# Kernel tuning notes

Hardware: AMD Instinct MI355X
Metric: run time of the kernel (lower is better)

Reference implementation:

```python
import jax, jax.numpy as jnp
import numpy as np

B, T, C, H = 16, 2048, 512, 64


def _skew(x):
    # x: (B, T1, T2) -> relative-position skew trick (Music Transformer)
    b, t1, t2 = x.shape
    x = jnp.pad(x, ((0, 0), (0, 0), (1, 0)))        # pad one column on the left
    x = x.reshape(b, t2 + 1, t1)                    # reinterpret layout
    x = x[:, 1:, :]                                 # drop first row
    return jnp.transpose(x, (0, 2, 1))              # (B, T1, T2)


def setup_inputs() -> dict:
    key = jax.random.key(0)
    ks = jax.random.split(key, 5)
    return {
        "x": jax.random.normal(ks[0], (B, T, C), dtype=jnp.float32),
        "Wq": jax.random.normal(ks[1], (C, H), dtype=jnp.float32) * 0.02,
        "Wk": jax.random.normal(ks[2], (C, H), dtype=jnp.float32) * 0.02,
        "Wv": jax.random.normal(ks[3], (C, H), dtype=jnp.float32) * 0.02,
        "Er": jax.random.normal(ks[4], (T, H), dtype=jnp.float32),
    }


def reference(x, Wq, Wk, Wv, Er):
    b, t, c = x.shape
    q = x @ Wq  # (B, T, H)
    k = x @ Wk
    v = x @ Wv
    scale = 1.0 / (k.shape[-1] ** 0.5)
    att = jnp.einsum("bth,bsh->bts", q, k) * scale  # (B, T, T)
    # relative position bias via skew trick
    rel_att = jnp.einsum("bth,rh->btr", q, Er[:t])  # (B, T, T)
    att = att + _skew(rel_att)
    # causal mask
    mask = jnp.tril(jnp.ones((t, t), dtype=bool))
    att = jnp.where(mask, att, -jnp.inf)
    att = jax.nn.softmax(att, axis=-1)
    # dropout is identity in eval mode
    out = att @ v  # (B, T, H)
    return out
```

## Files before the change

kernel.cpp:

```cpp
#include <hip/hip_runtime.h>
#include <hip/hip_bf16.h>

#define TT 2048
#define HB 64
#define NB 16
#define NSPLIT 6

typedef __attribute__((ext_vector_type(8))) short short8;
typedef __attribute__((ext_vector_type(4))) float floatx4;

static __device__ __forceinline__ unsigned short f2bf(float f) {
  __hip_bfloat16 h = __float2bfloat16(f);
  return *reinterpret_cast<unsigned short*>(&h);
}
static __device__ __forceinline__ float bf2f(unsigned short u) {
  __hip_bfloat16 h = *reinterpret_cast<__hip_bfloat16*>(&u);
  return __bfloat162float(h);
}

__global__ __launch_bounds__(256) void prep_kernel(
    const float* __restrict__ Wq, const float* __restrict__ Wk,
    const float* __restrict__ Wv, const float* __restrict__ Er,
    unsigned short* __restrict__ Wt, unsigned short* __restrict__ Erb) {
  const int bx = blockIdx.x, tid = threadIdx.x;
  if (bx < 512) {
    int idx = bx * 256 + tid;
    Erb[idx] = f2bf(Er[idx]);
  } else {
    int n = bx - 512;
    const float* Ws[3] = {Wq, Wk, Wv};
#pragma unroll
    for (int m = 0; m < 3; m++)
      for (int k = tid; k < 512; k += 256)
        Wt[(size_t)(m * 64 + n) * 512 + k] = f2bf(Ws[m][(size_t)k * 64 + n]);
  }
}

__global__ __launch_bounds__(256) void proj_kernel(
    const float* __restrict__ x, const unsigned short* __restrict__ Wt,
    unsigned short* __restrict__ qb, unsigned short* __restrict__ kb,
    unsigned short* __restrict__ vT) {
  const int tid = threadIdx.x;
  const int w = tid >> 6, l = tid & 63, quad = l >> 4, lm = l & 15;
  const int m0 = blockIdx.x * 64;
  const int row_a = m0 + w * 16 + lm;

  floatx4 acc[12];
#pragma unroll
  for (int i = 0; i < 12; i++) acc[i] = (floatx4){0.f, 0.f, 0.f, 0.f};

  auto LDA = [&](short8* af, int kt) {
#pragma unroll
    for (int kc = 0; kc < 2; kc++) {
      const float* px = &x[(size_t)row_a * 512 + kt + kc * 32 + quad * 8];
      float4 f0 = *(const float4*)px;
      float4 f1 = *(const float4*)(px + 4);
      short8 s;
      s[0] = f2bf(f0.x); s[1] = f2bf(f0.y); s[2] = f2bf(f0.z); s[3] = f2bf(f0.w);
      s[4] = f2bf(f1.x); s[5] = f2bf(f1.y); s[6] = f2bf(f1.z); s[7] = f2bf(f1.w);
      af[kc] = s;
    }
  };
  auto MFMAS = [&](const short8* af, int kt) {
#pragma unroll
    for (int nt = 0; nt < 12; nt++) {
      const unsigned short* pw =
          &Wt[(size_t)((nt >> 2) * 64 + (nt & 3) * 16 + lm) * 512 + kt + quad * 8];
      short8 b0 = *(const short8*)pw;
      short8 b1 = *(const short8*)(pw + 32);
      acc[nt] = __builtin_amdgcn_mfma_f32_16x16x32_bf16(af[0], b0, acc[nt], 0, 0, 0);
      acc[nt] = __builtin_amdgcn_mfma_f32_16x16x32_bf16(af[1], b1, acc[nt], 0, 0, 0);
    }
  };

  short8 afA[2], afB[2];
  LDA(afA, 0);
#pragma unroll
  for (int kt = 0; kt < 512; kt += 128) {
    LDA(afB, kt + 64);
    MFMAS(afA, kt);
    if (kt + 128 < 512) LDA(afA, kt + 128);
    MFMAS(afB, kt + 64);
  }

  const int b = m0 >> 11;
#pragma unroll
  for (int nt = 0; nt < 12; nt++) {
    int col = (nt & 3) * 16 + lm;
#pragma unroll
    for (int rg = 0; rg < 4; rg++) {
      int row = m0 + w * 16 + quad * 4 + rg;
      unsigned short hv = f2bf(acc[nt][rg]);
      if (nt < 4) qb[(size_t)row * 64 + col] = hv;
      else if (nt < 8) kb[(size_t)row * 64 + col] = hv;
      else vT[(size_t)(b * 64 + col) * 2048 + (row & 2047)] = hv;
    }
  }
}

#define SLICE_B 10880

__global__ __launch_bounds__(384, 2) void attn_kernel(
    const unsigned short* __restrict__ qb, const unsigned short* __restrict__ kb,
    const unsigned short* __restrict__ vT, const unsigned short* __restrict__ Erb,
    float* __restrict__ out) {
  __shared__ __align__(16) char smem[NSPLIT * SLICE_B];

  const int tid = threadIdx.x;
  const int w = tid >> 6;
  const int lane = tid & 63;
  const int quad = lane >> 4, lm = lane & 15;

  float* Ds = (float*)(smem + w * SLICE_B);
  unsigned short* Ps = (unsigned short*)(smem + w * SLICE_B + 8192);
  float* dbv = (float*)(smem + w * SLICE_B + 8192 + 2560);
  const float* DsL = Ds + lm * 63 + quad * 4;

  const int xcd = blockIdx.x & 7;
  const int slot = blockIdx.x >> 3;
  const int b = xcd + ((slot & 1) << 3);
  const int pr = slot >> 1;
  const int s = w;

  const size_t qoff = (size_t)b * (2048 * 64);
  const unsigned short* qB = qb + qoff;
  const unsigned short* kB = kb + qoff;
  const unsigned short* vB = vT + qoff;

  short8 ebf[2];
#pragma unroll
  for (int kc = 0; kc < 2; kc++) {
    short8 z = (short8){0, 0, 0, 0, 0, 0, 0, 0};
    if (lm == 0)
      z = *(const short8*)&Erb[(size_t)2047 * 64 + kc * 32 + quad * 8];
    ebf[kc] = z;
  }

  for (int ph = 0; ph < 2; ph++) {
    const int it = ph ? (63 - pr) : pr;
    const int i0 = it * 32;

    short8 qf[2][2];
#pragma unroll
    for (int mt = 0; mt < 2; mt++)
#pragma unroll
      for (int kc = 0; kc < 2; kc++)
        qf[mt][kc] =
            *(const short8*)&qB[(size_t)(i0 + mt * 16 + lm) * 64 + kc * 32 + quad * 8];

    if ((it % NSPLIT) == w) {
#pragma unroll
      for (int mt = 0; mt < 2; mt++) {
        floatx4 dacc = (floatx4){0.f, 0.f, 0.f, 0.f};
        dacc = __builtin_amdgcn_mfma_f32_16x16x32_bf16(qf[mt][0], ebf[0], dacc, 0, 0, 0);
        dacc = __builtin_amdgcn_mfma_f32_16x16x32_bf16(qf[mt][1], ebf[1], dacc, 0, 0, 0);
        if (lm == 0) {
#pragma unroll
          for (int rg = 0; rg < 4; rg++)
            dbv[mt * 16 + quad * 4 + rg] = dacc[rg];
        }
      }
    }
    __builtin_amdgcn_wave_barrier();

    floatx4 O[2][4];
#pragma unroll
    for (int mt = 0; mt < 2; mt++)
#pragma unroll
      for (int nt = 0; nt < 4; nt++) O[mt][nt] = (floatx4){0.f, 0.f, 0.f, 0.f};
    float m_st[2][4], l_st[2][4];
#pragma unroll
    for (int mt = 0; mt < 2; mt++)
#pragma unroll
      for (int rg = 0; rg < 4; rg++) { m_st[mt][rg] = -1e30f; l_st[mt][rg] = 0.f; }

    for (int jt = s; jt <= it; jt += NSPLIT) {
      const int j0 = jt * 32;
      const int d = i0 - j0;
      const int e0 = (d - 33 > 0) ? (d - 33) : 0;

      short8 kf[2][2], uf[2][2], ef[4][2], vf[4];
#pragma unroll
      for (int t = 0; t < 2; t++)
#pragma unroll
        for (int kc = 0; kc < 2; kc++)
          kf[t][kc] =
              *(const short8*)&kB[(size_t)(j0 + t * 16 + lm) * 64 + kc * 32 + quad * 8];
#pragma unroll
      for (int ct = 0; ct < 2; ct++)
#pragma unroll
        for (int kc = 0; kc < 2; kc++) {
          int ur = j0 + ct * 16 + lm + 1;
          if (ur > 2047) ur = 2047;
          uf[ct][kc] = *(const short8*)&qB[(size_t)ur * 64 + kc * 32 + quad * 8];
        }
#pragma unroll
      for (int et = 0; et < 4; et++)
#pragma unroll
        for (int kc = 0; kc < 2; kc++)
          ef[et][kc] = *(const short8*)&Erb[(size_t)(e0 + et * 16 + lm) * 64 +
                                            kc * 32 + quad * 8];
#pragma unroll
      for (int nt = 0; nt < 4; nt++)
        vf[nt] = *(const short8*)&vB[(size_t)(nt * 16 + lm) * 2048 + j0 + quad * 8];

      __builtin_amdgcn_wave_barrier();

#pragma unroll
      for (int ct = 0; ct < 2; ct++)
#pragma unroll
        for (int et = 0; et < 4; et++) {
          floatx4 dacc = (floatx4){0.f, 0.f, 0.f, 0.f};
          dacc = __builtin_amdgcn_mfma_f32_16x16x32_bf16(uf[ct][0], ef[et][0], dacc, 0, 0, 0);
          dacc = __builtin_amdgcn_mfma_f32_16x16x32_bf16(uf[ct][1], ef[et][1], dacc, 0, 0, 0);
#pragma unroll
          for (int rg = 0; rg < 4; rg++)
            Ds[(ct * 16 + quad * 4 + rg) * 64 + et * 16 + lm] = dacc[rg];
        }

      floatx4 S[2][2];
#pragma unroll
      for (int mt = 0; mt < 2; mt++)
#pragma unroll
        for (int t = 0; t < 2; t++) {
          floatx4 a = (floatx4){0.f, 0.f, 0.f, 0.f};
          a = __builtin_amdgcn_mfma_f32_16x16x32_bf16(qf[mt][0], kf[t][0], a, 0, 0, 0);
          a = __builtin_amdgcn_mfma_f32_16x16x32_bf16(qf[mt][1], kf[t][1], a, 0, 0, 0);
          S[mt][t] = a;
        }

      __builtin_amdgcn_wave_barrier();
      asm volatile("s_waitcnt lgkmcnt(0)" ::: "memory");
      __builtin_amdgcn_sched_barrier(0);

      float sv0[8], sv1[8], lmx[8];
      bool allok = true;
      if (d >= 64) {
#pragma unroll
        for (int mt = 0; mt < 2; mt++)
#pragma unroll
          for (int rg = 0; rg < 4; rg++) {
            const int c = mt * 4 + rg;
            float d0 = DsL[mt * 16 + rg + 31];
            float d1 = DsL[1008 + mt * 16 + rg + 31];
            sv0[c] = fmaf(0.125f, S[mt][0][rg], d0);
            sv1[c] = fmaf(0.125f, S[mt][1][rg], d1);
            lmx[c] = fmaxf(sv0[c], sv1[c]);
            allok = allok && (lmx[c] <= m_st[mt][rg] + 8.f);
          }
      } else {
#pragma unroll
        for (int mt = 0; mt < 2; mt++)
#pragma unroll
          for (int rg = 0; rg < 4; rg++) {
            const int c = mt * 4 + rg;
            const int rloc = mt * 16 + quad * 4 + rg;
            const int i = i0 + rloc;
            float v0, v1;
            {
              int j = j0 + lm;
              float raw = 0.125f * S[mt][0][rg];
              if (j > i) v0 = -1e30f;
              else if (j == i) v0 = raw + dbv[rloc];
              else if (j == i - 1) v0 = raw;
              else v0 = raw + Ds[lm * 64 + (i - j - 2 - e0)];
            }
            {
              int j = j0 + 16 + lm;
              float raw = 0.125f * S[mt][1][rg];
              if (j > i) v1 = -1e30f;
              else if (j == i) v1 = raw + dbv[rloc];
              else if (j == i - 1) v1 = raw;
              else v1 = raw + Ds[(16 + lm) * 64 + (i - j - 2 - e0)];
            }
            sv0[c] = v0; sv1[c] = v1;
            lmx[c] = fmaxf(v0, v1);
            allok = allok && (lmx[c] <= m_st[mt][rg] + 8.f);
          }
      }

      if (__all((int)allok)) {
#pragma unroll
        for (int mt = 0; mt < 2; mt++)
#pragma unroll
          for (int rg = 0; rg < 4; rg++) {
            const int c = mt * 4 + rg;
            const int rloc = mt * 16 + quad * 4 + rg;
            float p0 = __expf(sv0[c] - m_st[mt][rg]);
            float p1 = __expf(sv1[c] - m_st[mt][rg]);
            l_st[mt][rg] += p0 + p1;
            Ps[rloc * 40 + lm] = f2bf(p0);
            Ps[rloc * 40 + 16 + lm] = f2bf(p1);
          }
      } else {
#pragma unroll
        for (int mt = 0; mt < 2; mt++)
#pragma unroll
          for (int rg = 0; rg < 4; rg++) {
            const int c = mt * 4 + rg;
            const int rloc = mt * 16 + quad * 4 + rg;
            float mx = lmx[c];
            mx = fmaxf(mx, __shfl_xor(mx, 1));
            mx = fmaxf(mx, __shfl_xor(mx, 2));
            mx = fmaxf(mx, __shfl_xor(mx, 4));
            mx = fmaxf(mx, __shfl_xor(mx, 8));
            float m_new = fmaxf(m_st[mt][rg], mx);
            float alpha = __expf(m_st[mt][rg] - m_new);
            float p0 = __expf(sv0[c] - m_new);
            float p1 = __expf(sv1[c] - m_new);
            l_st[mt][rg] = l_st[mt][rg] * alpha + (p0 + p1);
            m_st[mt][rg] = m_new;
#pragma unroll
            for (int nt = 0; nt < 4; nt++) O[mt][nt][rg] *= alpha;
            Ps[rloc * 40 + lm] = f2bf(p0);
            Ps[rloc * 40 + 16 + lm] = f2bf(p1);
          }
      }

      __builtin_amdgcn_wave_barrier();
      asm volatile("s_waitcnt lgkmcnt(0)" ::: "memory");
      __builtin_amdgcn_sched_barrier(0);

#pragma unroll
      for (int mt = 0; mt < 2; mt++) {
        short8 pa = *(const short8*)&Ps[(mt * 16 + lm) * 40 + quad * 8];
#pragma unroll
        for (int nt = 0; nt < 4; nt++)
          O[mt][nt] = __builtin_amdgcn_mfma_f32_16x16x32_bf16(pa, vf[nt], O[mt][nt], 0, 0, 0);
      }
    }

    {
      float* Os = (float*)(smem + w * SLICE_B);
      float* mlm = (float*)(smem + w * SLICE_B + 8320);
      float* mll = (float*)(smem + w * SLICE_B + 8448);
#pragma unroll
      for (int mt = 0; mt < 2; mt++)
#pragma unroll
        for (int rg = 0; rg < 4; rg++) {
          float lr = l_st[mt][rg];
          lr += __shfl_xor(lr, 1);
          lr += __shfl_xor(lr, 2);
          lr += __shfl_xor(lr, 4);
          lr += __shfl_xor(lr, 8);
          const int rloc = mt * 16 + quad * 4 + rg;
          if (lm == 0) { mlm[rloc] = m_st[mt][rg]; mll[rloc] = lr; }
#pragma unroll
          for (int nt = 0; nt < 4; nt++)
            Os[rloc * 65 + nt * 16 + lm] = O[mt][nt][rg];
        }
    }
    __syncthreads();
    if (tid < 256) {
      const int row = tid >> 3, c0 = (tid & 7) * 8;
      float mstar = -1e30f;
#pragma unroll
      for (int s2 = 0; s2 < NSPLIT; s2++)
        mstar = fmaxf(mstar, *(const float*)(smem + s2 * SLICE_B + 8320 + row * 4));
      float den = 0.f;
      float acc[8];
#pragma unroll
      for (int c = 0; c < 8; c++) acc[c] = 0.f;
#pragma unroll
      for (int s2 = 0; s2 < NSPLIT; s2++) {
        const char* sl = smem + s2 * SLICE_B;
        float ms = *(const float*)(sl + 8320 + row * 4);
        float ls = *(const float*)(sl + 8448 + row * 4);
        float a = __expf(ms - mstar);
        den += a * ls;
        const float* osp = (const float*)sl + row * 65 + c0;
#pragma unroll
        for (int c = 0; c < 8; c++) acc[c] += a * osp[c];
      }
      float inv = 1.f / den;
      float4 r0 = {acc[0] * inv, acc[1] * inv, acc[2] * inv, acc[3] * inv};
      float4 r1 = {acc[4] * inv, acc[5] * inv, acc[6] * inv, acc[7] * inv};
      float* po = &out[qoff + (size_t)(i0 + row) * 64 + c0];
      *(float4*)po = r0;
      *((float4*)po + 1) = r1;
    }
    __syncthreads();
  }
}

extern "C" void kernel_launch(void* const* d_in, const int* in_sizes, int n_in,
                              void* d_out, int out_size, void* d_ws,
                              size_t ws_size, hipStream_t stream) {
  const float* x = (const float*)d_in[0];
  const float* Wq = (const float*)d_in[1];
  const float* Wk = (const float*)d_in[2];
  const float* Wv = (const float*)d_in[3];
  const float* Er = (const float*)d_in[4];
  float* out = (float*)d_out;

  unsigned short* qb = (unsigned short*)d_ws;
  unsigned short* kb = qb + 2097152;
  unsigned short* vT = kb + 2097152;
  unsigned short* Wt = vT + 2097152;
  unsigned short* Erb = Wt + 98304;

  prep_kernel<<<576, 256, 0, stream>>>(Wq, Wk, Wv, Er, Wt, Erb);
  proj_kernel<<<512, 256, 0, stream>>>(x, Wt, qb, kb, vT);
  attn_kernel<<<512, 384, 0, stream>>>(qb, kb, vT, Erb, out);
}
```

Baseline: 244.3 us.

## Store relative-bias tile in fp16 and merge splits in two halves to shrink LDS

The per-wave relative-position tile in shared memory is now stored as fp16 instead of fp32. The final cross-split merge of partial outputs is done in two 32-column halves, with an extra barrier between them. Together these cut the per-wave LDS slice from 10880 to 6784 bytes, which may allow more blocks per CU or reduce LDS traffic. The cost is fp16 rounding on the bias values, extra conversion instructions, and an additional synchronisation round in the epilogue.

```diff
diff --git a/kernel.cpp b/kernel.cpp
--- a/kernel.cpp
+++ b/kernel.cpp
@@ -1,5 +1,6 @@
 #include <hip/hip_runtime.h>
 #include <hip/hip_bf16.h>
+#include <hip/hip_fp16.h>
 
 #define TT 2048
 #define HB 64
@@ -16,6 +17,14 @@
 static __device__ __forceinline__ float bf2f(unsigned short u) {
   __hip_bfloat16 h = *reinterpret_cast<__hip_bfloat16*>(&u);
   return __bfloat162float(h);
+}
+static __device__ __forceinline__ unsigned short f2h(float f) {
+  __half h = __float2half(f);
+  return *reinterpret_cast<unsigned short*>(&h);
+}
+static __device__ __forceinline__ float h2f(unsigned short u) {
+  __half h = *reinterpret_cast<__half*>(&u);
+  return __half2float(h);
 }
 
 __global__ __launch_bounds__(256) void prep_kernel(
@@ -98,7 +107,7 @@
   }
 }
 
-#define SLICE_B 10880
+#define SLICE_B 6784
 
 __global__ __launch_bounds__(384, 2) void attn_kernel(
     const unsigned short* __restrict__ qb, const unsigned short* __restrict__ kb,
@@ -111,10 +120,10 @@
   const int lane = tid & 63;
   const int quad = lane >> 4, lm = lane & 15;
 
-  float* Ds = (float*)(smem + w * SLICE_B);
-  unsigned short* Ps = (unsigned short*)(smem + w * SLICE_B + 8192);
-  float* dbv = (float*)(smem + w * SLICE_B + 8192 + 2560);
-  const float* DsL = Ds + lm * 63 + quad * 4;
+  unsigned short* Dsb = (unsigned short*)(smem + w * SLICE_B);
+  unsigned short* Ps = (unsigned short*)(smem + w * SLICE_B + 4096);
+  float* dbv = (float*)(smem + w * SLICE_B + 6656);
+  const unsigned short* DsL16 = Dsb + lm * 63 + quad * 4;
 
   const int xcd = blockIdx.x & 7;
   const int slot = blockIdx.x >> 3;
@@ -215,7 +224,7 @@
           dacc = __builtin_amdgcn_mfma_f32_16x16x32_bf16(uf[ct][1], ef[et][1], dacc, 0, 0, 0);
 #pragma unroll
           for (int rg = 0; rg < 4; rg++)
-            Ds[(ct * 16 + quad * 4 + rg) * 64 + et * 16 + lm] = dacc[rg];
+            Dsb[(ct * 16 + quad * 4 + rg) * 64 + et * 16 + lm] = f2h(dacc[rg]);
         }
 
       floatx4 S[2][2];
@@ -241,8 +250,8 @@
 #pragma unroll
           for (int rg = 0; rg < 4; rg++) {
             const int c = mt * 4 + rg;
-            float d0 = DsL[mt * 16 + rg + 31];
-            float d1 = DsL[1008 + mt * 16 + rg + 31];
+            float d0 = h2f(DsL16[mt * 16 + rg + 31]);
+            float d1 = h2f(DsL16[1008 + mt * 16 + rg + 31]);
             sv0[c] = fmaf(0.125f, S[mt][0][rg], d0);
             sv1[c] = fmaf(0.125f, S[mt][1][rg], d1);
             lmx[c] = fmaxf(sv0[c], sv1[c]);
@@ -263,7 +272,7 @@
               if (j > i) v0 = -1e30f;
               else if (j == i) v0 = raw + dbv[rloc];
               else if (j == i - 1) v0 = raw;
-              else v0 = raw + Ds[lm * 64 + (i - j - 2 - e0)];
+              else v0 = raw + h2f(Dsb[lm * 64 + (i - j - 2 - e0)]);
             }
             {
               int j = j0 + 16 + lm;
@@ -271,7 +280,7 @@
               if (j > i) v1 = -1e30f;
               else if (j == i) v1 = raw + dbv[rloc];
               else if (j == i - 1) v1 = raw;
-              else v1 = raw + Ds[(16 + lm) * 64 + (i - j - 2 - e0)];
+              else v1 = raw + h2f(Dsb[(16 + lm) * 64 + (i - j - 2 - e0)]);
             }
             sv0[c] = v0; sv1[c] = v1;
             lmx[c] = fmaxf(v0, v1);
@@ -330,56 +339,64 @@
       }
     }
 
-    {
-      float* Os = (float*)(smem + w * SLICE_B);
-      float* mlm = (float*)(smem + w * SLICE_B + 8320);
-      float* mll = (float*)(smem + w * SLICE_B + 8448);
-#pragma unroll
-      for (int mt = 0; mt < 2; mt++)
-#pragma unroll
-        for (int rg = 0; rg < 4; rg++) {
-          float lr = l_st[mt][rg];
-          lr += __shfl_xor(lr, 1);
-          lr += __shfl_xor(lr, 2);
-          lr += __shfl_xor(lr, 4);
-          lr += __shfl_xor(lr, 8);
-          const int rloc = mt * 16 + quad * 4 + rg;
-          if (lm == 0) { mlm[rloc] = m_st[mt][rg]; mll[rloc] = lr; }
-#pragma unroll
-          for (int nt = 0; nt < 4; nt++)
-            Os[rloc * 65 + nt * 16 + lm] = O[mt][nt][rg];
+    float lred[2][4];
+#pragma unroll
+    for (int mt = 0; mt < 2; mt++)
+#pragma unroll
+      for (int rg = 0; rg < 4; rg++) {
+        float lr = l_st[mt][rg];
+        lr += __shfl_xor(lr, 1);
+        lr += __shfl_xor(lr, 2);
+        lr += __shfl_xor(lr, 4);
+        lr += __shfl_xor(lr, 8);
+        lred[mt][rg] = lr;
+      }
+#pragma unroll
+    for (int half = 0; half < 2; half++) {
+      {
+        float* Os = (float*)(smem + w * SLICE_B);
+        float* mlm = (float*)(smem + w * SLICE_B + 4608);
+        float* mll = (float*)(smem + w * SLICE_B + 4736);
+#pragma unroll
+        for (int mt = 0; mt < 2; mt++)
+#pragma unroll
+          for (int rg = 0; rg < 4; rg++) {
+            const int rloc = mt * 16 + quad * 4 + rg;
+            if (half == 0 && lm == 0) {
+              mlm[rloc] = m_st[mt][rg];
+              mll[rloc] = lred[mt][rg];
+            }
+#pragma unroll
+            for (int ntl = 0; ntl < 2; ntl++)
+              Os[rloc * 36 + ntl * 16 + lm] = O[mt][half * 2 + ntl][rg];
+          }
+      }
+      __syncthreads();
+      if (tid < 256) {
+        const int row = tid >> 3, c0 = (tid & 7) * 4;
+        float mstar = -1e30f;
+#pragma unroll
+        for (int s2 = 0; s2 < NSPLIT; s2++)
+          mstar = fmaxf(mstar, *(const float*)(smem + s2 * SLICE_B + 4608 + row * 4));
+        float den = 0.f;
+        float acc[4] = {0.f, 0.f, 0.f, 0.f};
+#pragma unroll
+        for (int s2 = 0; s2 < NSPLIT; s2++) {
+          const char* sl = smem + s2 * SLICE_B;
+          float ms = *(const float*)(sl + 4608 + row * 4);
+          float ls = *(const float*)(sl + 4736 + row * 4);
+          float a = __expf(ms - mstar);
+          den += a * ls;
+          const float* osp = (const float*)sl + row * 36 + c0;
+#pragma unroll
+          for (int c = 0; c < 4; c++) acc[c] += a * osp[c];
         }
-    }
-    __syncthreads();
-    if (tid < 256) {
-      const int row = tid >> 3, c0 = (tid & 7) * 8;
-      float mstar = -1e30f;
-#pragma unroll
-      for (int s2 = 0; s2 < NSPLIT; s2++)
-        mstar = fmaxf(mstar, *(const float*)(smem + s2 * SLICE_B + 8320 + row * 4));
-      float den = 0.f;
-      float acc[8];
-#pragma unroll
-      for (int c = 0; c < 8; c++) acc[c] = 0.f;
-#pragma unroll
-      for (int s2 = 0; s2 < NSPLIT; s2++) {
-        const char* sl = smem + s2 * SLICE_B;
-        float ms = *(const float*)(sl + 8320 + row * 4);
-        float ls = *(const float*)(sl + 8448 + row * 4);
-        float a = __expf(ms - mstar);
-        den += a * ls;
-        const float* osp = (const float*)sl + row * 65 + c0;
-#pragma unroll
-        for (int c = 0; c < 8; c++) acc[c] += a * osp[c];
-      }
-      float inv = 1.f / den;
-      float4 r0 = {acc[0] * inv, acc[1] * inv, acc[2] * inv, acc[3] * inv};
-      float4 r1 = {acc[4] * inv, acc[5] * inv, acc[6] * inv, acc[7] * inv};
-      float* po = &out[qoff + (size_t)(i0 + row) * 64 + c0];
-      *(float4*)po = r0;
-      *((float4*)po + 1) = r1;
-    }
-    __syncthreads();
+        float inv = 1.f / den;
+        float4 r = {acc[0] * inv, acc[1] * inv, acc[2] * inv, acc[3] * inv};
+        *(float4*)&out[qoff + (size_t)(i0 + row) * 64 + half * 32 + c0] = r;
+      }
+      __syncthreads();
+    }
   }
 }
 
```

After: 245.5 us. No clear change (+0.5%).
